# Performance work log

Measured on AMD Instinct MI355X. Metric: run time of the kernel, lower is better.

Reference implementation:

```python
import jax, jax.numpy as jnp
import numpy as np

# dims
C = 16      # input_channels
H = 64      # hidden_channels
HID = 128   # CDEFunc hidden width (hardcoded in source)
OUT = 1     # output_channels
L = 128     # number of time knots -> L-1 spline segments
B = 2048    # batch


def setup_inputs() -> dict:
    key = jax.random.key(0)
    ks = jax.random.split(key, 9)
    n = lambda k, shape, s: (jax.random.normal(k, shape, dtype=jnp.float32) * s)
    return {
        # cubic Hermite spline coeffs: concat(a, b, two_c, three_d) along last dim
        "coeffs": n(ks[0], (B, L - 1, 4 * C), 0.1),
        "W_init": n(ks[1], (H, C), 0.2),
        "b_init": jnp.zeros((H,), jnp.float32),
        "W1": n(ks[2], (HID, H), 0.1),
        "b1": jnp.zeros((HID,), jnp.float32),
        "W2": n(ks[3], (H * C, HID), 0.05),
        "b2": jnp.zeros((H * C,), jnp.float32),
        "W_out": n(ks[4], (OUT, H), 0.1),
        "b_out": jnp.zeros((OUT,), jnp.float32),
    }


def _spline_deriv(coeffs, t):
    """dX/dt of cubic spline at scalar time t. coeffs: (B, L-1, 4C)."""
    idx = jnp.clip(jnp.floor(t).astype(jnp.int32), 0, L - 2)
    seg = jax.lax.dynamic_slice_in_dim(coeffs, idx, 1, axis=1)[:, 0]  # (B, 4C)
    a, b, two_c, three_d = jnp.split(seg, 4, axis=-1)
    fr = t - idx.astype(t.dtype) if hasattr(t, 'dtype') else t - idx
    return b + two_c * fr + three_d * (fr * fr)  # (B, C)


def reference(coeffs, W_init, b_init, W1, b1, W2, b2, W_out, b_out):
    # X(0) = a of first segment (frac = 0)
    X0 = coeffs[:, 0, :C]
    z0 = X0 @ W_init.T + b_init  # (B, H)

    def f(z, dX):
        # CDEFunc: linear-relu-linear-tanh -> (B, H, C), then contract with dX/dt
        h = jax.nn.relu(z @ W1.T + b1)
        g = jnp.tanh(h @ W2.T + b2).reshape(-1, H, C)
        return jnp.einsum('bhc,bc->bh', g, dX)

    dt = jnp.float32(1.0)  # one RK4 step per knot interval

    def step(z, t):
        d0 = _spline_deriv(coeffs, t)
        dm = _spline_deriv(coeffs, t + 0.5 * dt)
        d1 = _spline_deriv(coeffs, t + dt)
        k1 = f(z, d0)
        k2 = f(z + 0.5 * dt * k1, dm)
        k3 = f(z + 0.5 * dt * k2, dm)
        k4 = f(z + dt * k3, d1)
        return z + (dt / 6.0) * (k1 + 2.0 * k2 + 2.0 * k3 + k4), None

    ts = jnp.arange(L - 1, dtype=jnp.float32)
    zT, _ = jax.lax.scan(step, z0, ts)
    return zT @ W_out.T + b_out  # (B, OUT)
```

## Files before the change

kernel.cpp:

```cpp
#include <hip/hip_runtime.h>

#define L_DIM 128
#define BB 8

typedef _Float16 f16;
typedef _Float16 f16x8 __attribute__((ext_vector_type(8)));
typedef float f32x4 __attribute__((ext_vector_type(4)));

__device__ __forceinline__ float fast_tanh_b(float x, float bk) {
    float e = __builtin_amdgcn_exp2f(fmaf(x, 2.8853900817779268f, bk));
    float r = __builtin_amdgcn_rcpf(e + 1.0f);
    return fmaf(-2.0f, r, 1.0f);
}

__attribute__((amdgpu_flat_work_group_size(512, 512), amdgpu_waves_per_eu(2)))
__global__ void
cde_kernel(const float* __restrict__ coeffs,
           const float* __restrict__ W_init, const float* __restrict__ b_init,
           const float* __restrict__ W1, const float* __restrict__ b1,
           const float* __restrict__ W2, const float* __restrict__ b2,
           const float* __restrict__ W_out, const float* __restrict__ b_out,
           float* __restrict__ out)
{
    __shared__ __align__(16) f16   z16[16][72];
    __shared__ __align__(16) f16   h16[16][136];
    __shared__ __align__(16) float dxT[2][3][16][20];
    __shared__ __align__(16) float zf[BB][64];

    const int tid  = threadIdx.x;
    const int blk  = blockIdx.x;
    const int lane = tid & 63;
    const int w    = tid >> 6;
    const int q    = lane >> 4;
    const int lr   = lane & 15;
    const int hh   = w * 8 + (lr & 7);
    const int chp  = lr >> 3;
    const int row0 = (q & 1) * 4 + (q >> 1) * 2;

    f16x8 w2f[8][4];
    float b2k[8];
#pragma unroll
    for (int t8 = 0; t8 < 8; ++t8) {
        const int outc = hh * 16 + 2 * t8 + chp;
        b2k[t8] = 2.8853900817779268f * b2[outc];
#pragma unroll
        for (int kc = 0; kc < 4; ++kc) {
            const float* src = W2 + (size_t)outc * 128 + kc * 32 + q * 8;
            f16x8 v;
#pragma unroll
            for (int i = 0; i < 8; ++i) v[i] = (f16)src[i];
            w2f[t8][kc] = v;
        }
    }
    f16x8 w1f[2];
#pragma unroll
    for (int kc = 0; kc < 2; ++kc) {
        const float* src = W1 + (size_t)(w * 16 + lr) * 64 + kc * 32 + q * 8;
        f16x8 v;
#pragma unroll
        for (int i = 0; i < 8; ++i) v[i] = (f16)src[i];
        w1f[kc] = v;
    }
    const float b1r = b1[w * 16 + lr];

    float z32r[2], ksumr[2];
#pragma unroll
    for (int j = 0; j < 2; ++j) {
        const float* x0 = coeffs + (size_t)(blk * BB + row0 + j) * (L_DIM - 1) * 64;
        float a = b_init[hh];
#pragma unroll
        for (int c = 0; c < 16; ++c) a = fmaf(x0[c], W_init[hh * 16 + c], a);
        z32r[j] = a;
        ksumr[j] = 0.f;
        if (lr < 8) z16[row0 + j][hh] = (f16)a;
    }
    for (int i = tid; i < 8 * 72; i += 512) z16[8 + i / 72][i % 72] = (f16)0.f;
    if (tid < BB * 16) {
        const int b = tid >> 4, c = tid & 15;
        const float* seg = coeffs + (size_t)(blk * BB + b) * (L_DIM - 1) * 64;
        float bv = seg[16 + c], cv = seg[32 + c], dv = seg[48 + c];
        dxT[0][0][c][b] = bv;
        dxT[0][1][c][b] = fmaf(0.25f, dv, fmaf(0.5f, cv, bv));
        dxT[0][2][c][b] = seg[64 + 16 + c];
    }
    __syncthreads();

    for (int t = 0; t < L_DIM - 1; ++t) {
        const int buf = t & 1;
        float pb = 0.f, pc = 0.f, pd = 0.f, pe = 0.f;
#pragma unroll
        for (int s = 0; s < 4; ++s) {
            {
                f16x8 za0 = *(const f16x8*)&z16[lr][q * 8];
                f16x8 za1 = *(const f16x8*)&z16[lr][32 + q * 8];
                f32x4 hacc = {0.f, 0.f, 0.f, 0.f};
                hacc = __builtin_amdgcn_mfma_f32_16x16x32_f16(za0, w1f[0], hacc, 0, 0, 0);
                hacc = __builtin_amdgcn_mfma_f32_16x16x32_f16(za1, w1f[1], hacc, 0, 0, 0);
#pragma unroll
                for (int r = 0; r < 4; ++r)
                    h16[q * 4 + r][w * 16 + lr] = (f16)fmaxf(hacc[r] + b1r, 0.f);
            }
            __syncthreads();

            const int ds = (s + 1) >> 1;
            float ka0 = 0.f, ka1 = 0.f;
#pragma unroll
            for (int hf = 0; hf < 2; ++hf) {
                float2 dvv[4];
#pragma unroll
                for (int tt = 0; tt < 4; ++tt)
                    dvv[tt] = *(const float2*)&dxT[buf][ds][2 * (hf * 4 + tt) + chp][row0];
                f32x4 acc[4];
#pragma unroll
                for (int tt = 0; tt < 4; ++tt)
                    acc[tt] = (f32x4){0.f, 0.f, 0.f, 0.f};
                if (w & 1) __builtin_amdgcn_s_setprio(1);
#pragma unroll
                for (int kc = 0; kc < 4; ++kc) {
                    f16x8 af = *(const f16x8*)&h16[lr][kc * 32 + q * 8];
#pragma unroll
                    for (int tt = 0; tt < 4; ++tt)
                        acc[tt] = __builtin_amdgcn_mfma_f32_16x16x32_f16(af, w2f[hf * 4 + tt][kc], acc[tt], 0, 0, 0);
                }
                if (w & 1) __builtin_amdgcn_s_setprio(0);
                if (hf == 0 && s == 1 && t < L_DIM - 2 && tid < 128) {
                    const int b = tid >> 4, c = tid & 15;
                    const float* seg = coeffs + ((size_t)(blk * BB + b) * (L_DIM - 1) + (t + 1)) * 64;
                    pb = seg[16 + c]; pc = seg[32 + c]; pd = seg[48 + c];
                    pe = (t + 1 < L_DIM - 2) ? seg[80 + c] : 0.f;
                }
#pragma unroll
                for (int tt = 0; tt < 4; ++tt) {
                    float u0 = __shfl_xor(acc[tt][2], 32);
                    float u1 = __shfl_xor(acc[tt][3], 32);
                    float g0 = fast_tanh_b((lane < 32) ? acc[tt][0] : u0, b2k[hf * 4 + tt]);
                    float g1 = fast_tanh_b((lane < 32) ? acc[tt][1] : u1, b2k[hf * 4 + tt]);
                    ka0 = fmaf(g0, dvv[tt].x, ka0);
                    ka1 = fmaf(g1, dvv[tt].y, ka1);
                }
            }
            ka0 += __shfl_xor(ka0, 8);
            ka1 += __shfl_xor(ka1, 8);
            float zs0, zs1;
            if (s == 3) {
                z32r[0] = fmaf(ksumr[0] + ka0, 1.f / 6.f, z32r[0]); zs0 = z32r[0];
                z32r[1] = fmaf(ksumr[1] + ka1, 1.f / 6.f, z32r[1]); zs1 = z32r[1];
            } else {
                ksumr[0] = (s == 0) ? ka0 : fmaf(2.f, ka0, ksumr[0]);
                ksumr[1] = (s == 0) ? ka1 : fmaf(2.f, ka1, ksumr[1]);
                const float alpha = (s == 2) ? 1.f : 0.5f;
                zs0 = fmaf(alpha, ka0, z32r[0]);
                zs1 = fmaf(alpha, ka1, z32r[1]);
            }
            if (lr < 8) {
                z16[row0 + 0][hh] = (f16)zs0;
                z16[row0 + 1][hh] = (f16)zs1;
            }
            if (s == 3 && t < L_DIM - 2 && tid < 128) {
                const int b = tid >> 4, c = tid & 15;
                dxT[buf ^ 1][0][c][b] = pb;
                dxT[buf ^ 1][1][c][b] = fmaf(0.25f, pd, fmaf(0.5f, pc, pb));
                dxT[buf ^ 1][2][c][b] = (t + 1 < L_DIM - 2) ? pe : (pb + pc + pd);
            }
            __syncthreads();
        }
    }

    if (lr < 8) {
        zf[row0 + 0][hh] = z32r[0];
        zf[row0 + 1][hh] = z32r[1];
    }
    __syncthreads();
    if (tid < 64) {
        const int b = lane >> 3, j0 = lane & 7;
        float p = 0.f;
#pragma unroll
        for (int m = 0; m < 8; ++m) p += zf[b][j0 + 8 * m] * W_out[j0 + 8 * m];
        p += __shfl_xor(p, 1, 64);
        p += __shfl_xor(p, 2, 64);
        p += __shfl_xor(p, 4, 64);
        if (j0 == 0) out[blk * BB + b] = p + b_out[0];
    }
}

extern "C" void kernel_launch(void* const* d_in, const int* in_sizes, int n_in,
                              void* d_out, int out_size, void* d_ws, size_t ws_size,
                              hipStream_t stream) {
    const float* coeffs = (const float*)d_in[0];
    const float* W_init = (const float*)d_in[1];
    const float* b_init = (const float*)d_in[2];
    const float* W1     = (const float*)d_in[3];
    const float* b1     = (const float*)d_in[4];
    const float* W2     = (const float*)d_in[5];
    const float* b2     = (const float*)d_in[6];
    const float* W_out  = (const float*)d_in[7];
    const float* b_out  = (const float*)d_in[8];
    cde_kernel<<<256, 512, 0, stream>>>(coeffs, W_init, b_init, W1, b1, W2, b2,
                                        W_out, b_out, (float*)d_out);
}
```

Measured before the change: 755.4 us.

## Compute full hidden layer redundantly per wave to drop a block barrier

Each wave now computes the whole 128-wide hidden activation itself, with W1 and b1 staged in shared memory and the operands swapped, and writes it into a private per-wave h16 slice. This removes one __syncthreads per RK stage, replacing it with a local LDS waitcnt. The cost is 8x redundant first-layer MFMA work, extra LDS reads of W1, and a larger shared-memory footprint. It also removes the setprio hints, stops unrolling the stage loop, and moves the next-segment prefetch to a different stage.

```diff
diff --git a/kernel.cpp b/kernel.cpp
--- a/kernel.cpp
+++ b/kernel.cpp
@@ -4,6 +4,7 @@
 #define BB 8
 
 typedef _Float16 f16;
+typedef _Float16 f16x4 __attribute__((ext_vector_type(4)));
 typedef _Float16 f16x8 __attribute__((ext_vector_type(8)));
 typedef float f32x4 __attribute__((ext_vector_type(4)));
 
@@ -23,7 +24,9 @@
            float* __restrict__ out)
 {
     __shared__ __align__(16) f16   z16[16][72];
-    __shared__ __align__(16) f16   h16[16][136];
+    __shared__ __align__(16) f16   w1l[8][2][64][8];
+    __shared__ __align__(16) float b1l[128];
+    __shared__ __align__(16) f16   h16p[8][16][136];
     __shared__ __align__(16) float dxT[2][3][16][20];
     __shared__ __align__(16) float zf[BB][64];
 
@@ -52,16 +55,12 @@
             w2f[t8][kc] = v;
         }
     }
-    f16x8 w1f[2];
-#pragma unroll
-    for (int kc = 0; kc < 2; ++kc) {
-        const float* src = W1 + (size_t)(w * 16 + lr) * 64 + kc * 32 + q * 8;
-        f16x8 v;
-#pragma unroll
-        for (int i = 0; i < 8; ++i) v[i] = (f16)src[i];
-        w1f[kc] = v;
-    }
-    const float b1r = b1[w * 16 + lr];
+#pragma unroll
+    for (int kc = 0; kc < 2; ++kc)
+#pragma unroll
+        for (int i = 0; i < 8; ++i)
+            w1l[w][kc][lane][i] = (f16)W1[(size_t)(w * 16 + lr) * 64 + kc * 32 + q * 8 + i];
+    if (tid < 128) b1l[tid] = b1[tid];
 
     float z32r[2], ksumr[2];
 #pragma unroll
@@ -88,19 +87,25 @@
     for (int t = 0; t < L_DIM - 1; ++t) {
         const int buf = t & 1;
         float pb = 0.f, pc = 0.f, pd = 0.f, pe = 0.f;
-#pragma unroll
         for (int s = 0; s < 4; ++s) {
-            {
-                f16x8 za0 = *(const f16x8*)&z16[lr][q * 8];
-                f16x8 za1 = *(const f16x8*)&z16[lr][32 + q * 8];
-                f32x4 hacc = {0.f, 0.f, 0.f, 0.f};
-                hacc = __builtin_amdgcn_mfma_f32_16x16x32_f16(za0, w1f[0], hacc, 0, 0, 0);
-                hacc = __builtin_amdgcn_mfma_f32_16x16x32_f16(za1, w1f[1], hacc, 0, 0, 0);
-#pragma unroll
-                for (int r = 0; r < 4; ++r)
-                    h16[q * 4 + r][w * 16 + lr] = (f16)fmaxf(hacc[r] + b1r, 0.f);
-            }
-            __syncthreads();
+            const f16x8 za0 = *(const f16x8*)&z16[lr][q * 8];
+            const f16x8 za1 = *(const f16x8*)&z16[lr][32 + q * 8];
+#pragma unroll
+            for (int n = 0; n < 8; ++n) {
+                const f16x8 a0 = *(const f16x8*)&w1l[n][0][lane][0];
+                const f16x8 a1 = *(const f16x8*)&w1l[n][1][lane][0];
+                const f32x4 bq = *(const f32x4*)&b1l[n * 16 + 4 * q];
+                f32x4 hc = {0.f, 0.f, 0.f, 0.f};
+                hc = __builtin_amdgcn_mfma_f32_16x16x32_f16(a0, za0, hc, 0, 0, 0);
+                hc = __builtin_amdgcn_mfma_f32_16x16x32_f16(a1, za1, hc, 0, 0, 0);
+                f16x4 pp;
+                pp[0] = (f16)fmaxf(hc[0] + bq[0], 0.f);
+                pp[1] = (f16)fmaxf(hc[1] + bq[1], 0.f);
+                pp[2] = (f16)fmaxf(hc[2] + bq[2], 0.f);
+                pp[3] = (f16)fmaxf(hc[3] + bq[3], 0.f);
+                *(f16x4*)&h16p[w][lr][n * 16 + 4 * q] = pp;
+            }
+            asm volatile("s_waitcnt lgkmcnt(0)" ::: "memory");
 
             const int ds = (s + 1) >> 1;
             float ka0 = 0.f, ka1 = 0.f;
@@ -114,16 +119,14 @@
 #pragma unroll
                 for (int tt = 0; tt < 4; ++tt)
                     acc[tt] = (f32x4){0.f, 0.f, 0.f, 0.f};
-                if (w & 1) __builtin_amdgcn_s_setprio(1);
 #pragma unroll
                 for (int kc = 0; kc < 4; ++kc) {
-                    f16x8 af = *(const f16x8*)&h16[lr][kc * 32 + q * 8];
+                    const f16x8 af = *(const f16x8*)&h16p[w][lr][kc * 32 + q * 8];
 #pragma unroll
                     for (int tt = 0; tt < 4; ++tt)
                         acc[tt] = __builtin_amdgcn_mfma_f32_16x16x32_f16(af, w2f[hf * 4 + tt][kc], acc[tt], 0, 0, 0);
                 }
-                if (w & 1) __builtin_amdgcn_s_setprio(0);
-                if (hf == 0 && s == 1 && t < L_DIM - 2 && tid < 128) {
+                if (hf == 0 && s == 2 && t < L_DIM - 2 && tid < 128) {
                     const int b = tid >> 4, c = tid & 15;
                     const float* seg = coeffs + ((size_t)(blk * BB + b) * (L_DIM - 1) + (t + 1)) * 64;
                     pb = seg[16 + c]; pc = seg[32 + c]; pd = seg[48 + c];
```

Measured after the change: 975.8 us. +29.2%, slower.
